# Kernel optimization log

Hardware: AMD Instinct MI355X
Metric: run time of the kernel (lower is better)

The kernel has to match this reference:

```python
import jax, jax.numpy as jnp
import numpy as np

B, C_IN, C_QKV, N = 8, 12, 36, 4096

def setup_inputs() -> dict:
    key = jax.random.key(0)
    ks = jax.random.split(key, 9)
    s_in = 1.0 / np.sqrt(C_IN)
    s_o = 1.0 / np.sqrt(C_QKV)
    return {
        "x": jax.random.normal(ks[0], (B, C_IN, N), dtype=jnp.float32),
        "wq": jax.random.uniform(ks[1], (C_QKV, C_IN), jnp.float32, -s_in, s_in),
        "bq": jax.random.uniform(ks[2], (C_QKV,), jnp.float32, -s_in, s_in),
        "wk": jax.random.uniform(ks[3], (C_QKV, C_IN), jnp.float32, -s_in, s_in),
        "bk": jax.random.uniform(ks[4], (C_QKV,), jnp.float32, -s_in, s_in),
        "wv": jax.random.uniform(ks[5], (C_QKV, C_IN), jnp.float32, -s_in, s_in),
        "bv": jax.random.uniform(ks[6], (C_QKV,), jnp.float32, -s_in, s_in),
        "wo": jax.random.uniform(ks[7], (C_IN, C_QKV), jnp.float32, -s_o, s_o),
        "bo": jax.random.uniform(ks[8], (C_IN,), jnp.float32, -s_o, s_o),
    }

def _conv1x1(w, b, x):
    # 1x1 Conv1d == channel-mixing matmul: [o,i] @ [b,i,n] -> [b,o,n]
    return jnp.einsum('oi,bin->bon', w, x) + b[None, :, None]

def reference(x, wq, bq, wk, bk, wv, bv, wo, bo):
    scale = 1.0 / jnp.sqrt(jnp.float32(x.shape[1]))  # 1/sqrt(12)
    q = _conv1x1(wq, bq, x)  # [B, 36, N]
    k = _conv1x1(wk, bk, x)
    v = _conv1x1(wv, bv, x)
    # inter = k^T @ q : scores[b,n,m] = sum_c k[b,c,n] * q[b,c,m]
    scores = jnp.einsum('bcn,bcm->bnm', k, q) * scale  # [B, N, N]
    weights = jax.nn.softmax(scores, axis=-1)
    attn = jnp.einsum('bcn,bnm->bcm', v, weights)  # v @ weights, [B, 36, N]
    return _conv1x1(wo, bo, attn)  # [B, 12, N]
```

## Files before the change

### kernel.cpp

```cpp
#include <hip/hip_runtime.h>
#include <hip/hip_bf16.h>
#include <math.h>

#define B 8
#define CIN 12
#define CQ 36
#define CP 48
#define N 4096
#define SCALE 0.28867513459481287f
#define LOG2E 1.4426950408889634f
#define ZSPLIT 8
#define NCHUNK (N / ZSPLIT)
#define NT (NCHUNK / 32)
#define MSPLIT 2

typedef __attribute__((ext_vector_type(4)))  short bf4_t;
typedef __attribute__((ext_vector_type(8)))  short bf8_t;
typedef __attribute__((ext_vector_type(16))) float f32x16;
typedef __attribute__((ext_vector_type(4)))  float f32x4;

__device__ __forceinline__ unsigned short f2bf(float x) {
  unsigned int u = __float_as_uint(x);
  u += 0x7FFFu + ((u >> 16) & 1u);
  return (unsigned short)(u >> 16);
}

#if __has_builtin(__builtin_amdgcn_cvt_pk_bf16_f32)
typedef __attribute__((ext_vector_type(2))) __bf16 bf16x2_t;
__device__ __forceinline__ unsigned pk2bf(float a, float b) {
  bf16x2_t v = __builtin_amdgcn_cvt_pk_bf16_f32(a, b);
  return __builtin_bit_cast(unsigned, v);
}
#else
__device__ __forceinline__ unsigned pk2bf(float a, float b) {
  return (__float_as_uint(a) >> 16) | (__float_as_uint(b) & 0xFFFF0000u);
}
#endif

__device__ __forceinline__ float bf2f(unsigned short u) {
  return __uint_as_float((unsigned)u << 16);
}

__device__ __forceinline__ float exp2fast(float x) {
#if __has_builtin(__builtin_amdgcn_exp2f)
  return __builtin_amdgcn_exp2f(x);
#else
  return exp2f(x);
#endif
}

__device__ __forceinline__ f32x4 mfma16(bf4_t a, bf4_t b, f32x4 c) {
#if __has_builtin(__builtin_amdgcn_mfma_f32_16x16x16bf16_1k)
  return __builtin_amdgcn_mfma_f32_16x16x16bf16_1k(a, b, c, 0, 0, 0);
#else
  bf8_t a8 = {a[0], a[1], a[2], a[3], 0, 0, 0, 0};
  bf8_t b8 = {b[0], b[1], b[2], b[3], 0, 0, 0, 0};
  return __builtin_amdgcn_mfma_f32_16x16x32_bf16(a8, b8, c, 0, 0, 0);
#endif
}

__device__ __forceinline__ bf8_t lds_bf8(const unsigned short* p) {
  uint2 a = *(const uint2*)p;
  uint2 b = *(const uint2*)(p + 4);
  uint4 r{a.x, a.y, b.x, b.y};
  return __builtin_bit_cast(bf8_t, r);
}
__device__ __forceinline__ void wlds16(unsigned short* p, uint4 v) {
  *(uint2*)p = uint2{v.x, v.y};
  *(uint2*)(p + 4) = uint2{v.z, v.w};
}

__global__ __launch_bounds__(256) void qkv_kernel(
    const float* __restrict__ x,
    const float* __restrict__ wq, const float* __restrict__ bq,
    const float* __restrict__ wk, const float* __restrict__ bk,
    const float* __restrict__ wv, const float* __restrict__ bv,
    const float* __restrict__ bo,
    unsigned short* __restrict__ qT, unsigned short* __restrict__ kT,
    unsigned short* __restrict__ vbf, float* __restrict__ out) {
  __shared__ float sw[CQ * CIN];
  __shared__ float sb[CQ];
  int z = blockIdx.y;
  int tid = threadIdx.x;
  if (z == 3) {
#pragma unroll
    for (int r = 0; r < 3; ++r) {
      int gid4 = blockIdx.x * 256 + tid + r * 32768;
      int e4 = gid4 * 4;
      int i = (e4 >> 12) % CIN;
      float bvv = bo[i];
      *(float4*)(out + e4) = float4{bvv, bvv, bvv, bvv};
    }
    return;
  }
  const float* w  = (z == 0) ? wq : (z == 1) ? wk : wv;
  const float* bb = (z == 0) ? bq : (z == 1) ? bk : bv;
  float scale = (z == 1) ? SCALE * LOG2E : 1.0f;
  for (int e = tid; e < CQ * CIN; e += 256) sw[e] = w[e] * scale;
  if (tid < CQ) sb[tid] = bb[tid] * scale;
  __syncthreads();
  int gid = blockIdx.x * 256 + tid;
  int b = gid >> 12;
  int n = gid & (N - 1);
  float xv[CIN];
#pragma unroll
  for (int i = 0; i < CIN; ++i) xv[i] = x[(b * CIN + i) * N + n];
  if (z == 2) {
#pragma unroll
    for (int o = 0; o < CQ; ++o) {
      float a = sb[o];
#pragma unroll
      for (int i = 0; i < CIN; ++i) a += sw[o * CIN + i] * xv[i];
      vbf[((size_t)b * CP + o) * N + n] = f2bf(a);
    }
  } else {
    __attribute__((aligned(16))) unsigned row[CP / 2];
#pragma unroll
    for (int o = 0; o < CQ; o += 2) {
      float a0 = sb[o], a1 = sb[o + 1];
#pragma unroll
      for (int i = 0; i < CIN; ++i) {
        float xi = xv[i];
        a0 += sw[o * CIN + i] * xi;
        a1 += sw[(o + 1) * CIN + i] * xi;
      }
      row[o / 2] = (unsigned)f2bf(a0) | ((unsigned)f2bf(a1) << 16);
    }
    row[18] = (z == 0) ? 0x3F803F80u : 0u;
#pragma unroll
    for (int o = 19; o < CP / 2; ++o) row[o] = 0;
    unsigned short* dst = ((z == 0) ? qT : kT) + ((size_t)b * N + n) * CP;
#pragma unroll
    for (int i = 0; i < 6; ++i) *(uint4*)(dst + 8 * i) = *(const uint4*)&row[4 * i];
  }
}

__global__ __launch_bounds__(256) void stats_kernel(
    const unsigned short* __restrict__ qT, const unsigned short* __restrict__ kT,
    float* __restrict__ psum) {
  __shared__ float red[4][64];
  int tid = threadIdx.x, lane = tid & 63, wave = tid >> 6;
  int b = blockIdx.y, nblk = blockIdx.x, ms = blockIdx.z;
  int l31 = lane & 31, h = lane >> 5;
  int n0 = nblk * 64;
  size_t bN = (size_t)b * N;
  const unsigned short* krow0 = kT + (bN + n0 + l31) * CP + h * 8;
  const unsigned short* krow1 = krow0 + (size_t)32 * CP;
  bf8_t a0 = *(const bf8_t*)(krow0);
  bf8_t a1 = *(const bf8_t*)(krow0 + 16);
  bf8_t a2 = *(const bf8_t*)(krow0 + 32);
  bf8_t a3 = *(const bf8_t*)(krow1);
  bf8_t a4 = *(const bf8_t*)(krow1 + 16);
  bf8_t a5 = *(const bf8_t*)(krow1 + 32);
  float rs0[16], rs1[16];
#pragma unroll
  for (int r = 0; r < 16; ++r) { rs0[r] = 0.f; rs1[r] = 0.f; }
  const int MW = N / MSPLIT / 4;
  const unsigned short* qbase =
      qT + (bN + ms * (N / MSPLIT) + wave * MW + l31) * CP + h * 8;
#pragma unroll 2
  for (int t = 0; t < MW / 32; ++t) {
    const unsigned short* qrow2 = qbase + (size_t)t * 32 * CP;
    bf8_t b0 = *(const bf8_t*)(qrow2);
    bf8_t b1 = *(const bf8_t*)(qrow2 + 16);
    bf8_t b2 = *(const bf8_t*)(qrow2 + 32);
    f32x16 S0, S1;
#pragma unroll
    for (int r = 0; r < 16; ++r) { S0[r] = 0.f; S1[r] = 0.f; }
    S0 = __builtin_amdgcn_mfma_f32_32x32x16_bf16(a0, b0, S0, 0, 0, 0);
    S0 = __builtin_amdgcn_mfma_f32_32x32x16_bf16(a1, b1, S0, 0, 0, 0);
    S0 = __builtin_amdgcn_mfma_f32_32x32x16_bf16(a2, b2, S0, 0, 0, 0);
    S1 = __builtin_amdgcn_mfma_f32_32x32x16_bf16(a3, b0, S1, 0, 0, 0);
    S1 = __builtin_amdgcn_mfma_f32_32x32x16_bf16(a4, b1, S1, 0, 0, 0);
    S1 = __builtin_amdgcn_mfma_f32_32x32x16_bf16(a5, b2, S1, 0, 0, 0);
#pragma unroll
    for (int r = 0; r < 16; ++r) {
      rs0[r] += exp2fast(S0[r]);
      rs1[r] += exp2fast(S1[r]);
    }
  }
#pragma unroll
  for (int off = 16; off >= 1; off >>= 1)
#pragma unroll
    for (int r = 0; r < 16; ++r) {
      rs0[r] += __shfl_xor(rs0[r], off, 32);
      rs1[r] += __shfl_xor(rs1[r], off, 32);
    }
  if (l31 == 0) {
#pragma unroll
    for (int r = 0; r < 16; ++r) {
      int row = (r & 3) + 8 * (r >> 2) + 4 * h;
      red[wave][row] = rs0[r];
      red[wave][32 + row] = rs1[r];
    }
  }
  __syncthreads();
  if (tid < 64) {
    float s = red[0][tid] + red[1][tid] + red[2][tid] + red[3][tid];
    psum[((size_t)ms * B + b) * N + n0 + tid] = s;
  }
}

__global__ __launch_bounds__(256, 3) void attn_kernel(
    const unsigned short* __restrict__ qT, const unsigned short* __restrict__ kT,
    const unsigned short* __restrict__ vbf, const float* __restrict__ wo,
    const float* __restrict__ psum, float* __restrict__ out) {
  __shared__ unsigned short kbuf[2][32 * 52];
  __shared__ unsigned short vbuf[2][48 * 36];
  __shared__ unsigned short plds[4][2][32 * 40];
  int tid = threadIdx.x, lane = tid & 63, wave = tid >> 6;
  int b = blockIdx.y, z = blockIdx.z, mblk = blockIdx.x;
  int l31 = lane & 31, h = lane >> 5, l15 = lane & 15, q4 = lane >> 4;
  int m0 = mblk * 256 + wave * 64;
  size_t bN = (size_t)b * N;
  bool isK0 = tid < 192;
  int r0row = isK0 ? (tid / 6) : ((tid - 192) >> 2);
  int r0c   = isK0 ? (tid % 6) : ((tid - 192) & 3);
  const unsigned short* s0 = isK0
      ? kT + (bN + z * NCHUNK + r0row) * CP + r0c * 8
      : vbf + ((size_t)b * CP + r0row) * N + z * NCHUNK + r0c * 8;
  int s0stride = isK0 ? 32 * CP : 32;
  unsigned short* dst0 = isK0 ? &kbuf[0][r0row * 52 + r0c * 8]
                              : &vbuf[0][r0row * 36 + r0c * 8];
  int dbs0 = isK0 ? 32 * 52 : 48 * 36;
  bool has1 = tid < 128;
  int r1row = (tid >> 2) + 16;
  int r1c = tid & 3;
  const unsigned short* s1 =
      vbf + ((size_t)b * CP + r1row) * N + z * NCHUNK + r1c * 8;
  unsigned short* dst1 = &vbuf[0][r1row * 36 + r1c * 8];
  const int dbs1 = 48 * 36;
  bool isP = isK0 && (r0c == 4);
  const float* pL = psum + bN + z * NCHUNK + r0row;
  bf8_t qb[2][3];
#pragma unroll
  for (int mt = 0; mt < 2; ++mt) {
    const unsigned short* qrow = qT + (bN + m0 + mt * 32 + l31) * CP + h * 8;
    qb[mt][0] = *(const bf8_t*)(qrow);
    qb[mt][1] = *(const bf8_t*)(qrow + 16);
    qb[mt][2] = *(const bf8_t*)(qrow + 32);
  }
  bf4_t woa[3];
#pragma unroll
  for (int ct = 0; ct < 3; ++ct) {
    float4 w4 = {0.f, 0.f, 0.f, 0.f};
    int col = 16 * ct + q4 * 4;
    if (l15 < CIN && col < CQ) w4 = *(const float4*)(wo + l15 * CQ + col);
    woa[ct] = bf4_t{(short)f2bf(w4.x), (short)f2bf(w4.y),
                    (short)f2bf(w4.z), (short)f2bf(w4.w)};
  }
  f32x4 acc[2][3][2];
#pragma unroll
  for (int mt = 0; mt < 2; ++mt)
#pragma unroll
    for (int ct = 0; ct < 3; ++ct)
#pragma unroll
      for (int hm = 0; hm < 2; ++hm)
#pragma unroll
        for (int r = 0; r < 4; ++r) acc[mt][ct][hm][r] = 0.f;
  uint4 r0 = *(const uint4*)s0; s0 += s0stride;
  uint4 r1{0, 0, 0, 0};
  if (has1) { r1 = *(const uint4*)s1; s1 += 32; }
  float Lp = 0.f;
  if (isP) { Lp = pL[0] + pL[(size_t)B * N]; pL += 32; }
  if (isP) {
    float tl = -__log2f(Lp);
    unsigned short hi = f2bf(tl);
    unsigned short lo = f2bf(tl - bf2f(hi));
    r0.z = (unsigned)hi | ((unsigned)lo << 16);
  }
  wlds16(dst0, r0);
  if (has1) wlds16(dst1, r1);
  __syncthreads();
  for (int t = 0; t < NT; ++t) {
    int buf = t & 1;
    if (t + 1 < NT) {
      r0 = *(const uint4*)s0; s0 += s0stride;
      if (has1) { r1 = *(const uint4*)s1; s1 += 32; }
      if (isP) { Lp = pL[0] + pL[(size_t)B * N]; pL += 32; }
    }
    const unsigned short* kb = kbuf[buf];
    const unsigned short* vb = vbuf[buf];
    bf8_t a0 = lds_bf8(kb + l31 * 52 + h * 8);
    bf8_t a1 = lds_bf8(kb + l31 * 52 + h * 8 + 16);
    bf8_t a2 = lds_bf8(kb + l31 * 52 + h * 8 + 32);
#pragma unroll
    for (int mt = 0; mt < 2; ++mt) {
      f32x16 S;
#pragma unroll
      for (int r = 0; r < 16; ++r) S[r] = 0.f;
      S = __builtin_amdgcn_mfma_f32_32x32x16_bf16(a0, qb[mt][0], S, 0, 0, 0);
      S = __builtin_amdgcn_mfma_f32_32x32x16_bf16(a1, qb[mt][1], S, 0, 0, 0);
      S = __builtin_amdgcn_mfma_f32_32x32x16_bf16(a2, qb[mt][2], S, 0, 0, 0);
      unsigned short* pl = plds[wave][mt];
#pragma unroll
      for (int qd = 0; qd < 4; ++qd) {
        uint2 pk;
        pk.x = pk2bf(exp2fast(S[4 * qd + 0]), exp2fast(S[4 * qd + 1]));
        pk.y = pk2bf(exp2fast(S[4 * qd + 2]), exp2fast(S[4 * qd + 3]));
        *(uint2*)&pl[l31 * 40 + 8 * qd + 4 * h] = pk;
      }
    }
    bf8_t v0 = lds_bf8(vb + (0 * 16 + l15) * 36 + q4 * 8);
    bf8_t v1 = lds_bf8(vb + (1 * 16 + l15) * 36 + q4 * 8);
    bf8_t v2 = lds_bf8(vb + (2 * 16 + l15) * 36 + q4 * 8);
#pragma unroll
    for (int mt = 0; mt < 2; ++mt) {
      const unsigned short* pl = plds[wave][mt];
      bf8_t pb0 = *(const bf8_t*)&pl[l15 * 40 + q4 * 8];
      bf8_t pb1 = *(const bf8_t*)&pl[(16 + l15) * 40 + q4 * 8];
      acc[mt][0][0] = __builtin_amdgcn_mfma_f32_16x16x32_bf16(v0, pb0, acc[mt][0][0], 0, 0, 0);
      acc[mt][0][1] = __builtin_amdgcn_mfma_f32_16x16x32_bf16(v0, pb1, acc[mt][0][1], 0, 0, 0);
      acc[mt][1][0] = __builtin_amdgcn_mfma_f32_16x16x32_bf16(v1, pb0, acc[mt][1][0], 0, 0, 0);
      acc[mt][1][1] = __builtin_amdgcn_mfma_f32_16x16x32_bf16(v1, pb1, acc[mt][1][1], 0, 0, 0);
      acc[mt][2][0] = __builtin_amdgcn_mfma_f32_16x16x32_bf16(v2, pb0, acc[mt][2][0], 0, 0, 0);
      acc[mt][2][1] = __builtin_amdgcn_mfma_f32_16x16x32_bf16(v2, pb1, acc[mt][2][1], 0, 0, 0);
    }
    if (t + 1 < NT) {
      int nb = buf ^ 1;
      if (isP) {
        float tl = -__log2f(Lp);
        unsigned short hi = f2bf(tl);
        unsigned short lo = f2bf(tl - bf2f(hi));
        r0.z = (unsigned)hi | ((unsigned)lo << 16);
      }
      wlds16(dst0 + nb * dbs0, r0);
      if (has1) wlds16(dst1 + nb * dbs1, r1);
    }
    __syncthreads();
  }
#pragma unroll
  for (int mt = 0; mt < 2; ++mt)
#pragma unroll
    for (int hm = 0; hm < 2; ++hm) {
      f32x4 po = {0.f, 0.f, 0.f, 0.f};
#pragma unroll
      for (int ct = 0; ct < 3; ++ct) {
        union { uint2 u; bf4_t v; } pb;
        pb.u.x = pk2bf(acc[mt][ct][hm][0], acc[mt][ct][hm][1]);
        pb.u.y = pk2bf(acc[mt][ct][hm][2], acc[mt][ct][hm][3]);
        po = mfma16(woa[ct], pb.v, po);
      }
      if (q4 < 3) {
        float* ob = out + ((size_t)b * CIN + q4 * 4) * N + m0 + mt * 32 + hm * 16 + l15;
#pragma unroll
        for (int r = 0; r < 4; ++r) atomicAdd(ob + (size_t)r * N, po[r]);
      }
    }
}

extern "C" void kernel_launch(void* const* d_in, const int* in_sizes, int n_in,
                              void* d_out, int out_size, void* d_ws, size_t ws_size,
                              hipStream_t stream) {
  const float* x  = (const float*)d_in[0];
  const float* wq = (const float*)d_in[1];
  const float* bq = (const float*)d_in[2];
  const float* wk = (const float*)d_in[3];
  const float* bk = (const float*)d_in[4];
  const float* wv = (const float*)d_in[5];
  const float* bv = (const float*)d_in[6];
  const float* wo = (const float*)d_in[7];
  const float* bo = (const float*)d_in[8];
  float* out = (float*)d_out;

  char* ws = (char*)d_ws;
  unsigned short* qT  = (unsigned short*)ws;
  unsigned short* kT  = (unsigned short*)(ws + 3145728);
  unsigned short* vbf = (unsigned short*)(ws + 2 * 3145728);
  float* psum = (float*)(ws + 3 * 3145728);

  qkv_kernel<<<dim3(B * N / 256, 4), 256, 0, stream>>>(x, wq, bq, wk, bk, wv, bv,
                                                       bo, qT, kT, vbf, out);
  stats_kernel<<<dim3(N / 64, B, MSPLIT), 256, 0, stream>>>(qT, kT, psum);
  attn_kernel<<<dim3(N / 256, B, ZSPLIT), 256, 0, stream>>>(qT, kT, vbf, wo, psum, out);
}
```

Measured before the change: 143.0 us.

## Preload whole K/V chunk into LDS once and drop per-tile double buffering

The attention kernel now loads its entire K/V chunk (256 keys with ZSPLIT doubled to 16) into LDS in a single prologue and then iterates over tiles without any per-iteration global loads or __syncthreads. This removes the per-tile barrier and the load/store pipeline of the old double-buffered scheme. The row-sum split is also raised to MSPLIT=4, so each block sums four partial sums when forming the log normaliser. The cost is more LDS per block (occupancy hint lowered from 3 to 2), an exposed prologue load with no overlap, and twice as many atomic adds to the output from the larger z-split.

```diff
diff --git a/kernel.cpp b/kernel.cpp
--- a/kernel.cpp
+++ b/kernel.cpp
@@ -9,10 +9,10 @@
 #define N 4096
 #define SCALE 0.28867513459481287f
 #define LOG2E 1.4426950408889634f
-#define ZSPLIT 8
+#define ZSPLIT 16
 #define NCHUNK (N / ZSPLIT)
 #define NT (NCHUNK / 32)
-#define MSPLIT 2
+#define MSPLIT 4
 
 typedef __attribute__((ext_vector_type(4)))  short bf4_t;
 typedef __attribute__((ext_vector_type(8)))  short bf8_t;
@@ -201,37 +201,59 @@
   }
 }
 
-__global__ __launch_bounds__(256, 3) void attn_kernel(
+__global__ __launch_bounds__(256, 2) void attn_kernel(
     const unsigned short* __restrict__ qT, const unsigned short* __restrict__ kT,
     const unsigned short* __restrict__ vbf, const float* __restrict__ wo,
     const float* __restrict__ psum, float* __restrict__ out) {
-  __shared__ unsigned short kbuf[2][32 * 52];
-  __shared__ unsigned short vbuf[2][48 * 36];
+  __shared__ unsigned short kbuf[NCHUNK * 52];
+  __shared__ unsigned short vbuf[48 * (NCHUNK + 4)];
   __shared__ unsigned short plds[4][2][32 * 40];
   int tid = threadIdx.x, lane = tid & 63, wave = tid >> 6;
   int b = blockIdx.y, z = blockIdx.z, mblk = blockIdx.x;
   int l31 = lane & 31, h = lane >> 5, l15 = lane & 15, q4 = lane >> 4;
   int m0 = mblk * 256 + wave * 64;
   size_t bN = (size_t)b * N;
-  bool isK0 = tid < 192;
-  int r0row = isK0 ? (tid / 6) : ((tid - 192) >> 2);
-  int r0c   = isK0 ? (tid % 6) : ((tid - 192) & 3);
-  const unsigned short* s0 = isK0
-      ? kT + (bN + z * NCHUNK + r0row) * CP + r0c * 8
-      : vbf + ((size_t)b * CP + r0row) * N + z * NCHUNK + r0c * 8;
-  int s0stride = isK0 ? 32 * CP : 32;
-  unsigned short* dst0 = isK0 ? &kbuf[0][r0row * 52 + r0c * 8]
-                              : &vbuf[0][r0row * 36 + r0c * 8];
-  int dbs0 = isK0 ? 32 * 52 : 48 * 36;
-  bool has1 = tid < 128;
-  int r1row = (tid >> 2) + 16;
-  int r1c = tid & 3;
-  const unsigned short* s1 =
-      vbf + ((size_t)b * CP + r1row) * N + z * NCHUNK + r1c * 8;
-  unsigned short* dst1 = &vbuf[0][r1row * 36 + r1c * 8];
-  const int dbs1 = 48 * 36;
-  bool isP = isK0 && (r0c == 4);
-  const float* pL = psum + bN + z * NCHUNK + r0row;
+  int n0 = z * NCHUNK;
+  uint4 sv[12];
+  const unsigned short* ksrc = kT + (bN + n0) * CP;
+#pragma unroll
+  for (int j = 0; j < 6; ++j) {
+    int idx = j * 256 + tid;
+    int row = idx / 6, c = idx % 6;
+    sv[j] = *(const uint4*)(ksrc + (size_t)row * CP + c * 8);
+  }
+#pragma unroll
+  for (int j = 0; j < 6; ++j) {
+    int vi = j * 256 + tid;
+    int row = vi >> 5, c = vi & 31;
+    sv[6 + j] = *(const uint4*)(vbf + ((size_t)b * CP + row) * N + n0 + c * 8);
+  }
+#pragma unroll
+  for (int j = 0; j < 6; ++j) {
+    int idx = j * 256 + tid;
+    int row = idx / 6, c = idx % 6;
+    if (c == 4) {
+      const float* pL = psum + bN + n0 + row;
+      float Lp = pL[0] + pL[(size_t)B * N] + pL[2 * (size_t)B * N] +
+                 pL[3 * (size_t)B * N];
+      float tl = -__log2f(Lp);
+      unsigned short hi = f2bf(tl);
+      unsigned short lo = f2bf(tl - bf2f(hi));
+      sv[j].z = (unsigned)hi | ((unsigned)lo << 16);
+    }
+  }
+#pragma unroll
+  for (int j = 0; j < 6; ++j) {
+    int idx = j * 256 + tid;
+    int row = idx / 6, c = idx % 6;
+    wlds16(&kbuf[row * 52 + c * 8], sv[j]);
+  }
+#pragma unroll
+  for (int j = 0; j < 6; ++j) {
+    int vi = j * 256 + tid;
+    int row = vi >> 5, c = vi & 31;
+    wlds16(&vbuf[row * (NCHUNK + 4) + c * 8], sv[6 + j]);
+  }
   bf8_t qb[2][3];
 #pragma unroll
   for (int mt = 0; mt < 2; ++mt) {
@@ -258,29 +280,10 @@
       for (int hm = 0; hm < 2; ++hm)
 #pragma unroll
         for (int r = 0; r < 4; ++r) acc[mt][ct][hm][r] = 0.f;
-  uint4 r0 = *(const uint4*)s0; s0 += s0stride;
-  uint4 r1{0, 0, 0, 0};
-  if (has1) { r1 = *(const uint4*)s1; s1 += 32; }
-  float Lp = 0.f;
-  if (isP) { Lp = pL[0] + pL[(size_t)B * N]; pL += 32; }
-  if (isP) {
-    float tl = -__log2f(Lp);
-    unsigned short hi = f2bf(tl);
-    unsigned short lo = f2bf(tl - bf2f(hi));
-    r0.z = (unsigned)hi | ((unsigned)lo << 16);
-  }
-  wlds16(dst0, r0);
-  if (has1) wlds16(dst1, r1);
   __syncthreads();
   for (int t = 0; t < NT; ++t) {
-    int buf = t & 1;
-    if (t + 1 < NT) {
-      r0 = *(const uint4*)s0; s0 += s0stride;
-      if (has1) { r1 = *(const uint4*)s1; s1 += 32; }
-      if (isP) { Lp = pL[0] + pL[(size_t)B * N]; pL += 32; }
-    }
-    const unsigned short* kb = kbuf[buf];
-    const unsigned short* vb = vbuf[buf];
+    const unsigned short* kb = kbuf + t * 32 * 52;
+    const unsigned short* vb = vbuf + t * 32;
     bf8_t a0 = lds_bf8(kb + l31 * 52 + h * 8);
     bf8_t a1 = lds_bf8(kb + l31 * 52 + h * 8 + 16);
     bf8_t a2 = lds_bf8(kb + l31 * 52 + h * 8 + 32);
@@ -301,9 +304,9 @@
         *(uint2*)&pl[l31 * 40 + 8 * qd + 4 * h] = pk;
       }
     }
-    bf8_t v0 = lds_bf8(vb + (0 * 16 + l15) * 36 + q4 * 8);
-    bf8_t v1 = lds_bf8(vb + (1 * 16 + l15) * 36 + q4 * 8);
-    bf8_t v2 = lds_bf8(vb + (2 * 16 + l15) * 36 + q4 * 8);
+    bf8_t v0 = lds_bf8(vb + (0 * 16 + l15) * (NCHUNK + 4) + q4 * 8);
+    bf8_t v1 = lds_bf8(vb + (1 * 16 + l15) * (NCHUNK + 4) + q4 * 8);
+    bf8_t v2 = lds_bf8(vb + (2 * 16 + l15) * (NCHUNK + 4) + q4 * 8);
 #pragma unroll
     for (int mt = 0; mt < 2; ++mt) {
       const unsigned short* pl = plds[wave][mt];
@@ -316,18 +319,6 @@
       acc[mt][2][0] = __builtin_amdgcn_mfma_f32_16x16x32_bf16(v2, pb0, acc[mt][2][0], 0, 0, 0);
       acc[mt][2][1] = __builtin_amdgcn_mfma_f32_16x16x32_bf16(v2, pb1, acc[mt][2][1], 0, 0, 0);
     }
-    if (t + 1 < NT) {
-      int nb = buf ^ 1;
-      if (isP) {
-        float tl = -__log2f(Lp);
-        unsigned short hi = f2bf(tl);
-        unsigned short lo = f2bf(tl - bf2f(hi));
-        r0.z = (unsigned)hi | ((unsigned)lo << 16);
-      }
-      wlds16(dst0 + nb * dbs0, r0);
-      if (has1) wlds16(dst1 + nb * dbs1, r1);
-    }
-    __syncthreads();
   }
 #pragma unroll
   for (int mt = 0; mt < 2; ++mt)
```

Result: slower. 151.6 us (+6.0%).

## Precompute log-normalizer into K buffer and load K fragments directly from global

Applied to the files above, without the earlier changes.

Adds a small prep kernel that combines the two partial softmax sums, takes -log2, and writes the hi/lo bf16 pair into the padding columns of kT. The attention kernel then drops its K shared-memory staging buffer and the in-loop log computation, reading K MFMA fragments straight from global (L2-resident) memory, while only V is staged through LDS. It also pads the P tile row stride to 44 to change the bank pattern, and raises the occupancy hint to 4 blocks per CU. The trade is an extra kernel launch and uncoalesced-ish direct global K loads inside the loop, whose latency is no longer hidden by the double buffer.

```diff
diff --git a/kernel.cpp b/kernel.cpp
--- a/kernel.cpp
+++ b/kernel.cpp
@@ -13,6 +13,7 @@
 #define NCHUNK (N / ZSPLIT)
 #define NT (NCHUNK / 32)
 #define MSPLIT 2
+#define PLD 44
 
 typedef __attribute__((ext_vector_type(4)))  short bf4_t;
 typedef __attribute__((ext_vector_type(8)))  short bf8_t;
@@ -201,37 +202,35 @@
   }
 }
 
-__global__ __launch_bounds__(256, 3) void attn_kernel(
+__global__ __launch_bounds__(256) void prep_kernel(
+    const float* __restrict__ psum, unsigned short* __restrict__ kT) {
+  int gid = blockIdx.x * 256 + threadIdx.x;
+  float L = psum[gid] + psum[B * N + gid];
+  float t = -__log2f(L);
+  unsigned short hi = f2bf(t);
+  unsigned short lo = f2bf(t - bf2f(hi));
+  *(unsigned*)(kT + (size_t)gid * CP + 36) = (unsigned)hi | ((unsigned)lo << 16);
+}
+
+__global__ __launch_bounds__(256, 4) void attn_kernel(
     const unsigned short* __restrict__ qT, const unsigned short* __restrict__ kT,
     const unsigned short* __restrict__ vbf, const float* __restrict__ wo,
-    const float* __restrict__ psum, float* __restrict__ out) {
-  __shared__ unsigned short kbuf[2][32 * 52];
+    float* __restrict__ out) {
   __shared__ unsigned short vbuf[2][48 * 36];
-  __shared__ unsigned short plds[4][2][32 * 40];
+  __shared__ unsigned short plds[4][2][32 * PLD];
   int tid = threadIdx.x, lane = tid & 63, wave = tid >> 6;
   int b = blockIdx.y, z = blockIdx.z, mblk = blockIdx.x;
   int l31 = lane & 31, h = lane >> 5, l15 = lane & 15, q4 = lane >> 4;
   int m0 = mblk * 256 + wave * 64;
   size_t bN = (size_t)b * N;
-  bool isK0 = tid < 192;
-  int r0row = isK0 ? (tid / 6) : ((tid - 192) >> 2);
-  int r0c   = isK0 ? (tid % 6) : ((tid - 192) & 3);
-  const unsigned short* s0 = isK0
-      ? kT + (bN + z * NCHUNK + r0row) * CP + r0c * 8
-      : vbf + ((size_t)b * CP + r0row) * N + z * NCHUNK + r0c * 8;
-  int s0stride = isK0 ? 32 * CP : 32;
-  unsigned short* dst0 = isK0 ? &kbuf[0][r0row * 52 + r0c * 8]
-                              : &vbuf[0][r0row * 36 + r0c * 8];
-  int dbs0 = isK0 ? 32 * 52 : 48 * 36;
-  bool has1 = tid < 128;
-  int r1row = (tid >> 2) + 16;
-  int r1c = tid & 3;
-  const unsigned short* s1 =
-      vbf + ((size_t)b * CP + r1row) * N + z * NCHUNK + r1c * 8;
-  unsigned short* dst1 = &vbuf[0][r1row * 36 + r1c * 8];
-  const int dbs1 = 48 * 36;
-  bool isP = isK0 && (r0c == 4);
-  const float* pL = psum + bN + z * NCHUNK + r0row;
+  int n0 = z * NCHUNK;
+  bool isV = tid < 192;
+  int vrow = tid >> 2, vc = tid & 3;
+  const unsigned short* vs =
+      vbf + ((size_t)b * CP + vrow) * N + n0 + vc * 8;
+  unsigned short* vdst = &vbuf[0][vrow * 36 + vc * 8];
+  const int vdbs = 48 * 36;
+  const unsigned short* kbase = kT + (bN + n0 + l31) * CP + h * 8;
   bf8_t qb[2][3];
 #pragma unroll
   for (int mt = 0; mt < 2; ++mt) {
@@ -258,32 +257,17 @@
       for (int hm = 0; hm < 2; ++hm)
 #pragma unroll
         for (int r = 0; r < 4; ++r) acc[mt][ct][hm][r] = 0.f;
-  uint4 r0 = *(const uint4*)s0; s0 += s0stride;
-  uint4 r1{0, 0, 0, 0};
-  if (has1) { r1 = *(const uint4*)s1; s1 += 32; }
-  float Lp = 0.f;
-  if (isP) { Lp = pL[0] + pL[(size_t)B * N]; pL += 32; }
-  if (isP) {
-    float tl = -__log2f(Lp);
-    unsigned short hi = f2bf(tl);
-    unsigned short lo = f2bf(tl - bf2f(hi));
-    r0.z = (unsigned)hi | ((unsigned)lo << 16);
-  }
-  wlds16(dst0, r0);
-  if (has1) wlds16(dst1, r1);
+  uint4 r0{0, 0, 0, 0};
+  if (isV) { r0 = *(const uint4*)vs; vs += 32; }
+  if (isV) wlds16(vdst, r0);
   __syncthreads();
   for (int t = 0; t < NT; ++t) {
     int buf = t & 1;
-    if (t + 1 < NT) {
-      r0 = *(const uint4*)s0; s0 += s0stride;
-      if (has1) { r1 = *(const uint4*)s1; s1 += 32; }
-      if (isP) { Lp = pL[0] + pL[(size_t)B * N]; pL += 32; }
-    }
-    const unsigned short* kb = kbuf[buf];
-    const unsigned short* vb = vbuf[buf];
-    bf8_t a0 = lds_bf8(kb + l31 * 52 + h * 8);
-    bf8_t a1 = lds_bf8(kb + l31 * 52 + h * 8 + 16);
-    bf8_t a2 = lds_bf8(kb + l31 * 52 + h * 8 + 32);
+    const unsigned short* kr = kbase + (size_t)t * 32 * CP;
+    bf8_t a0 = *(const bf8_t*)(kr);
+    bf8_t a1 = *(const bf8_t*)(kr + 16);
+    bf8_t a2 = *(const bf8_t*)(kr + 32);
+    if (t + 1 < NT && isV) { r0 = *(const uint4*)vs; vs += 32; }
 #pragma unroll
     for (int mt = 0; mt < 2; ++mt) {
       f32x16 S;
@@ -298,17 +282,18 @@
         uint2 pk;
         pk.x = pk2bf(exp2fast(S[4 * qd + 0]), exp2fast(S[4 * qd + 1]));
         pk.y = pk2bf(exp2fast(S[4 * qd + 2]), exp2fast(S[4 * qd + 3]));
-        *(uint2*)&pl[l31 * 40 + 8 * qd + 4 * h] = pk;
+        *(uint2*)&pl[l31 * PLD + 8 * qd + 4 * h] = pk;
       }
     }
+    const unsigned short* vb = vbuf[buf];
     bf8_t v0 = lds_bf8(vb + (0 * 16 + l15) * 36 + q4 * 8);
     bf8_t v1 = lds_bf8(vb + (1 * 16 + l15) * 36 + q4 * 8);
     bf8_t v2 = lds_bf8(vb + (2 * 16 + l15) * 36 + q4 * 8);
 #pragma unroll
     for (int mt = 0; mt < 2; ++mt) {
       const unsigned short* pl = plds[wave][mt];
-      bf8_t pb0 = *(const bf8_t*)&pl[l15 * 40 + q4 * 8];
-      bf8_t pb1 = *(const bf8_t*)&pl[(16 + l15) * 40 + q4 * 8];
+      bf8_t pb0 = *(const bf8_t*)&pl[l15 * PLD + q4 * 8];
+      bf8_t pb1 = *(const bf8_t*)&pl[(16 + l15) * PLD + q4 * 8];
       acc[mt][0][0] = __builtin_amdgcn_mfma_f32_16x16x32_bf16(v0, pb0, acc[mt][0][0], 0, 0, 0);
       acc[mt][0][1] = __builtin_amdgcn_mfma_f32_16x16x32_bf16(v0, pb1, acc[mt][0][1], 0, 0, 0);
       acc[mt][1][0] = __builtin_amdgcn_mfma_f32_16x16x32_bf16(v1, pb0, acc[mt][1][0], 0, 0, 0);
@@ -316,17 +301,7 @@
       acc[mt][2][0] = __builtin_amdgcn_mfma_f32_16x16x32_bf16(v2, pb0, acc[mt][2][0], 0, 0, 0);
       acc[mt][2][1] = __builtin_amdgcn_mfma_f32_16x16x32_bf16(v2, pb1, acc[mt][2][1], 0, 0, 0);
     }
-    if (t + 1 < NT) {
-      int nb = buf ^ 1;
-      if (isP) {
-        float tl = -__log2f(Lp);
-        unsigned short hi = f2bf(tl);
-        unsigned short lo = f2bf(tl - bf2f(hi));
-        r0.z = (unsigned)hi | ((unsigned)lo << 16);
-      }
-      wlds16(dst0 + nb * dbs0, r0);
-      if (has1) wlds16(dst1 + nb * dbs1, r1);
-    }
+    if (t + 1 < NT && isV) wlds16(vdst + (buf ^ 1) * vdbs, r0);
     __syncthreads();
   }
 #pragma unroll
@@ -372,5 +347,6 @@
   qkv_kernel<<<dim3(B * N / 256, 4), 256, 0, stream>>>(x, wq, bq, wk, bk, wv, bv,
                                                        bo, qT, kT, vbf, out);
   stats_kernel<<<dim3(N / 64, B, MSPLIT), 256, 0, stream>>>(qT, kT, psum);
-  attn_kernel<<<dim3(N / 256, B, ZSPLIT), 256, 0, stream>>>(qT, kT, vbf, wo, psum, out);
-}
+  prep_kernel<<<B * N / 256, 256, 0, stream>>>(psum, kT);
+  attn_kernel<<<dim3(N / 256, B, ZSPLIT), 256, 0, stream>>>(qT, kT, vbf, wo, out);
+}
```

Measured after the change: 153.7 us. 7.5% more time.

## Precompute log-normalizer in prep kernel, double split factors, pad P LDS stride

Applied to the files above, without the earlier changes.

Moves the per-row softmax normalizer (sum of split partial sums, negative log2, hi/lo bf16 split) out of the attention inner loop into a separate prep kernel that writes it into the kT padding columns. It also doubles the key split (ZSPLIT 8→16) and the stats split (MSPLIT 2→4) to raise parallelism, raises the launch-bounds occupancy hint to 4 blocks, and pads the P tile LDS row stride to cut bank conflicts. The cost is an extra kernel launch, more partial outputs to combine (presumably via atomic accumulation into out) and shorter per-block loops with more prologue/epilogue overhead.

```diff
diff --git a/kernel.cpp b/kernel.cpp
--- a/kernel.cpp
+++ b/kernel.cpp
@@ -9,10 +9,11 @@
 #define N 4096
 #define SCALE 0.28867513459481287f
 #define LOG2E 1.4426950408889634f
-#define ZSPLIT 8
+#define ZSPLIT 16
 #define NCHUNK (N / ZSPLIT)
 #define NT (NCHUNK / 32)
-#define MSPLIT 2
+#define MSPLIT 4
+#define PLD 44
 
 typedef __attribute__((ext_vector_type(4)))  short bf4_t;
 typedef __attribute__((ext_vector_type(8)))  short bf8_t;
@@ -201,13 +202,24 @@
   }
 }
 
-__global__ __launch_bounds__(256, 3) void attn_kernel(
+__global__ __launch_bounds__(256) void prep_kernel(
+    const float* __restrict__ psum, unsigned short* __restrict__ kT) {
+  int gid = blockIdx.x * 256 + threadIdx.x;
+  float L = psum[gid] + psum[B * N + gid] + psum[2 * B * N + gid] +
+            psum[3 * B * N + gid];
+  float t = -__log2f(L);
+  unsigned short hi = f2bf(t);
+  unsigned short lo = f2bf(t - bf2f(hi));
+  *(unsigned*)(kT + (size_t)gid * CP + 36) = (unsigned)hi | ((unsigned)lo << 16);
+}
+
+__global__ __launch_bounds__(256, 4) void attn_kernel(
     const unsigned short* __restrict__ qT, const unsigned short* __restrict__ kT,
     const unsigned short* __restrict__ vbf, const float* __restrict__ wo,
-    const float* __restrict__ psum, float* __restrict__ out) {
+    float* __restrict__ out) {
   __shared__ unsigned short kbuf[2][32 * 52];
   __shared__ unsigned short vbuf[2][48 * 36];
-  __shared__ unsigned short plds[4][2][32 * 40];
+  __shared__ unsigned short plds[4][2][32 * PLD];
   int tid = threadIdx.x, lane = tid & 63, wave = tid >> 6;
   int b = blockIdx.y, z = blockIdx.z, mblk = blockIdx.x;
   int l31 = lane & 31, h = lane >> 5, l15 = lane & 15, q4 = lane >> 4;
@@ -230,8 +242,6 @@
       vbf + ((size_t)b * CP + r1row) * N + z * NCHUNK + r1c * 8;
   unsigned short* dst1 = &vbuf[0][r1row * 36 + r1c * 8];
   const int dbs1 = 48 * 36;
-  bool isP = isK0 && (r0c == 4);
-  const float* pL = psum + bN + z * NCHUNK + r0row;
   bf8_t qb[2][3];
 #pragma unroll
   for (int mt = 0; mt < 2; ++mt) {
@@ -261,14 +271,6 @@
   uint4 r0 = *(const uint4*)s0; s0 += s0stride;
   uint4 r1{0, 0, 0, 0};
   if (has1) { r1 = *(const uint4*)s1; s1 += 32; }
-  float Lp = 0.f;
-  if (isP) { Lp = pL[0] + pL[(size_t)B * N]; pL += 32; }
-  if (isP) {
-    float tl = -__log2f(Lp);
-    unsigned short hi = f2bf(tl);
-    unsigned short lo = f2bf(tl - bf2f(hi));
-    r0.z = (unsigned)hi | ((unsigned)lo << 16);
-  }
   wlds16(dst0, r0);
   if (has1) wlds16(dst1, r1);
   __syncthreads();
@@ -277,7 +279,6 @@
     if (t + 1 < NT) {
       r0 = *(const uint4*)s0; s0 += s0stride;
       if (has1) { r1 = *(const uint4*)s1; s1 += 32; }
-      if (isP) { Lp = pL[0] + pL[(size_t)B * N]; pL += 32; }
     }
     const unsigned short* kb = kbuf[buf];
     const unsigned short* vb = vbuf[buf];
@@ -298,7 +299,7 @@
         uint2 pk;
         pk.x = pk2bf(exp2fast(S[4 * qd + 0]), exp2fast(S[4 * qd + 1]));
         pk.y = pk2bf(exp2fast(S[4 * qd + 2]), exp2fast(S[4 * qd + 3]));
-        *(uint2*)&pl[l31 * 40 + 8 * qd + 4 * h] = pk;
+        *(uint2*)&pl[l31 * PLD + 8 * qd + 4 * h] = pk;
       }
     }
     bf8_t v0 = lds_bf8(vb + (0 * 16 + l15) * 36 + q4 * 8);
@@ -307,8 +308,8 @@
 #pragma unroll
     for (int mt = 0; mt < 2; ++mt) {
       const unsigned short* pl = plds[wave][mt];
-      bf8_t pb0 = *(const bf8_t*)&pl[l15 * 40 + q4 * 8];
-      bf8_t pb1 = *(const bf8_t*)&pl[(16 + l15) * 40 + q4 * 8];
+      bf8_t pb0 = *(const bf8_t*)&pl[l15 * PLD + q4 * 8];
+      bf8_t pb1 = *(const bf8_t*)&pl[(16 + l15) * PLD + q4 * 8];
       acc[mt][0][0] = __builtin_amdgcn_mfma_f32_16x16x32_bf16(v0, pb0, acc[mt][0][0], 0, 0, 0);
       acc[mt][0][1] = __builtin_amdgcn_mfma_f32_16x16x32_bf16(v0, pb1, acc[mt][0][1], 0, 0, 0);
       acc[mt][1][0] = __builtin_amdgcn_mfma_f32_16x16x32_bf16(v1, pb0, acc[mt][1][0], 0, 0, 0);
@@ -318,12 +319,6 @@
     }
     if (t + 1 < NT) {
       int nb = buf ^ 1;
-      if (isP) {
-        float tl = -__log2f(Lp);
-        unsigned short hi = f2bf(tl);
-        unsigned short lo = f2bf(tl - bf2f(hi));
-        r0.z = (unsigned)hi | ((unsigned)lo << 16);
-      }
       wlds16(dst0 + nb * dbs0, r0);
       if (has1) wlds16(dst1 + nb * dbs1, r1);
     }
@@ -372,5 +367,6 @@
   qkv_kernel<<<dim3(B * N / 256, 4), 256, 0, stream>>>(x, wq, bq, wk, bk, wv, bv,
                                                        bo, qT, kT, vbf, out);
   stats_kernel<<<dim3(N / 64, B, MSPLIT), 256, 0, stream>>>(qT, kT, psum);
-  attn_kernel<<<dim3(N / 256, B, ZSPLIT), 256, 0, stream>>>(qT, kT, vbf, wo, psum, out);
-}
+  prep_kernel<<<B * N / 256, 256, 0, stream>>>(psum, kT);
+  attn_kernel<<<dim3(N / 256, B, ZSPLIT), 256, 0, stream>>>(qT, kT, vbf, wo, out);
+}
```

New measurement: 164.3 us. 14.9% more time.
